# Optimization experiments

Hardware: AMD Instinct MI355X
Metric: run time of the kernel (lower is better)

The kernel has to match this reference:

```python
import jax, jax.numpy as jnp
import numpy as np

TIME_GAP_BUCKETS = 64
B, L, H, MAX_T = 256, 200, 256, 256
VOCAB, N_GROUPS = 50000, 16
EPS = 1e-5


def setup_inputs() -> dict:
    key = jax.random.key(0)
    ks = jax.random.split(key, 16)
    lengths = jax.random.randint(ks[0], (B,), 0, L + 1)
    mask = jnp.arange(L)[None, :] < lengths[:, None]

    def toks(k, hi):  # jagged padded-dense: zeros past each row's length
        return jnp.where(mask, jax.random.randint(k, (B, L), 0, hi), 0)

    inp = {
        'history_tokens': toks(ks[1], VOCAB),
        'history_post_tokens': toks(ks[2], VOCAB),
        'history_author_tokens': toks(ks[3], VOCAB),
        'history_action_tokens': toks(ks[4], VOCAB),
        'history_time_gap': toks(ks[5], TIME_GAP_BUCKETS + 1),
        'history_group_ids': jnp.where(mask, jnp.sort(jax.random.randint(ks[6], (B, L), 1, N_GROUPS + 1), axis=1), 0),
        'lengths': lengths,
    }
    s = 0.02
    inp['token_emb'] = jax.random.normal(ks[7], (VOCAB, H)) * s
    inp['ln_gamma'] = jnp.ones((6 * H,))
    inp['ln_beta'] = jnp.zeros((6 * H,))
    inp['w1'] = jax.random.normal(ks[8], (6 * H, 4 * H)) * (1.0 / np.sqrt(6 * H)).astype(np.float32)
    inp['b1'] = jnp.zeros((4 * H,))
    inp['w2'] = jax.random.normal(ks[9], (4 * H, H)) * (1.0 / np.sqrt(4 * H)).astype(np.float32)
    inp['b2'] = jnp.zeros((H,))
    inp['time_gap_emb'] = (jax.random.normal(ks[10], (TIME_GAP_BUCKETS + 1, H)) * s).at[0].set(0.0)  # padding_idx=0
    inp['group_emb'] = (jax.random.normal(ks[11], (N_GROUPS + 1, H)) * s).at[0].set(0.0)  # padding_idx=0
    inp['pos_emb'] = jax.random.normal(ks[12], (MAX_T, H)) * s
    inp['sep_token'] = jax.random.normal(ks[13], (H,)) * 0.02
    return inp


def _layernorm(x, g, b):
    mu = jnp.mean(x, axis=-1, keepdims=True)
    var = jnp.mean(jnp.square(x - mu), axis=-1, keepdims=True)
    return (x - mu) * jax.lax.rsqrt(var + EPS) * g + b


def _merge_with_sep(event_tokens, group_ids, mask, sep_token):
    # mask is a prefix mask (positions < lengths), so valid tokens are contiguous.
    Bn, Ln, Hn = event_tokens.shape
    next_mask = jnp.pad(mask[:, 1:], ((0, 0), (0, 1)))
    next_group = jnp.pad(group_ids[:, 1:], ((0, 0), (0, 1)))
    sep_after = mask & next_mask & (group_ids != next_group)  # insert sep after token i
    seps_before = jnp.cumsum(sep_after, axis=1) - sep_after.astype(jnp.int32)  # exclusive scan
    token_pos = jnp.arange(Ln)[None, :] + seps_before  # position within merged piece list
    total = mask.sum(axis=1) + sep_after.sum(axis=1)  # [B] merged piece count
    offset = MAX_T - total  # right-align; negative -> leading pieces dropped
    tok_idx = offset[:, None] + token_pos
    sep_idx = tok_idx + 1
    tok_idx = jnp.where(mask & (tok_idx >= 0), tok_idx, MAX_T)  # MAX_T => dropped
    sep_idx = jnp.where(sep_after & (sep_idx >= 0), sep_idx, MAX_T)
    sep_rows = jnp.broadcast_to(sep_token, (Ln, Hn))

    def scatter_one(ev, ti, si):
        buf = jnp.zeros((MAX_T, Hn), ev.dtype)
        buf = buf.at[ti].set(ev, mode='drop')
        buf = buf.at[si].set(sep_rows, mode='drop')
        return buf

    merged = jax.vmap(scatter_one)(event_tokens, tok_idx, sep_idx)
    merged_len = jnp.minimum(total, MAX_T)
    merged_mask = jnp.arange(MAX_T)[None, :] >= (MAX_T - merged_len)[:, None]
    return merged, merged_mask


def reference(history_tokens, history_post_tokens, history_author_tokens,
              history_action_tokens, history_time_gap, history_group_ids,
              lengths, token_emb, ln_gamma, ln_beta, w1, b1, w2, b2,
              time_gap_emb, group_emb, pos_emb, sep_token):
    mask = jnp.arange(L)[None, :] < lengths[:, None]
    hh = token_emb[history_tokens]
    ph = token_emb[history_post_tokens]
    ah = token_emb[history_author_tokens]
    ch = token_emb[history_action_tokens]
    th = time_gap_emb[jnp.clip(history_time_gap, 0, TIME_GAP_BUCKETS)]
    gh = group_emb[history_group_ids]
    ev = jnp.concatenate([hh, ph, ah, ch, th, gh], axis=-1)  # [B, L, 6H]
    x = _layernorm(ev, ln_gamma, ln_beta)
    x = jax.nn.silu(x @ w1 + b1)  # dropout is identity in eval mode
    event_tokens = x @ w2 + b2  # [B, L, H]
    merged, mm = _merge_with_sep(event_tokens, history_group_ids, mask, sep_token)
    merged = (merged + pos_emb[None]) * mm[..., None].astype(merged.dtype)
    return merged, mm
```

## Files before the change

### kernel.cpp

```cpp
#include <hip/hip_runtime.h>
#include <hip/hip_bf16.h>
#include <math.h>

#define B_    256
#define L_    200
#define H_    256
#define MAXT  256
#define SIXH  1536
#define FOURH 1024
#define NPOS  (B_ * L_)

typedef __attribute__((ext_vector_type(8))) short short8;
typedef __attribute__((ext_vector_type(4))) float f32x4;

typedef __attribute__((address_space(3))) void lds_void;
typedef const __attribute__((address_space(1))) void gbl_void;

#define ASM_BAR() asm volatile("s_barrier" ::: "memory")
#define VMCNT4()  asm volatile("s_waitcnt vmcnt(4)" ::: "memory")
#define VMCNT0()  asm volatile("s_waitcnt vmcnt(0)" ::: "memory")

__global__ void scan_offsets(const int* __restrict__ lengths,
                             int* __restrict__ offsets) {
  if (threadIdx.x == 0) {
    int acc = 0;
    for (int b = 0; b < B_; b++) { offsets[b] = acc; acc += lengths[b]; }
    offsets[B_] = acc;
  }
}

__global__ void zero_pad_x(__hip_bfloat16* __restrict__ x,
                           const int* __restrict__ offsets) {
  int total = offsets[B_];
  int padded = (total + 255) & ~255;
  int row = total + blockIdx.x;
  if (row >= padded) return;
  int t = threadIdx.x;
#pragma unroll
  for (int j = 0; j < 6; j++)
    x[(size_t)row * SIXH + j * 256 + t] = __float2bfloat16(0.0f);
}

__global__ void tpos_kernel(const int* __restrict__ gids,
                            const int* __restrict__ lengths,
                            const int* __restrict__ offsets,
                            int* __restrict__ tpos) {
  int b = blockIdx.x;
  if (threadIdx.x != 0) return;
  int len = lengths[b];
  int base = offsets[b];
  const int* g = gids + b * L_;
  int nsep = 0;
  for (int l = 0; l + 1 < len; l++)
    if (g[l] != g[l + 1]) nsep++;
  int total = len + nsep;
  int off = MAXT - total;
  int sb = 0;
  for (int l = 0; l < len; l++) {
    int ti = off + l + sb;
    tpos[base + l] = (ti >= 0) ? (b * MAXT + ti) : -1;
    if (l + 1 < len && g[l] != g[l + 1]) sb++;
  }
}

__global__ void transpose_to_bf16(const float* __restrict__ in,
                                  __hip_bfloat16* __restrict__ out,
                                  int R, int C) {
  __shared__ float tile[32][33];
  int tc = blockIdx.x, tr = blockIdx.y;
  int tx = threadIdx.x & 31, ty = threadIdx.x >> 5;
#pragma unroll
  for (int i = 0; i < 4; i++) {
    int r = tr * 32 + ty + i * 8;
    int c = tc * 32 + tx;
    tile[ty + i * 8][tx] = in[(size_t)r * C + c];
  }
  __syncthreads();
#pragma unroll
  for (int i = 0; i < 4; i++) {
    int orow = tc * 32 + ty + i * 8;
    int ocol = tr * 32 + tx;
    out[(size_t)orow * R + ocol] = __float2bfloat16(tile[tx][ty + i * 8]);
  }
}

__global__ void embed_ln_kernel(const int* __restrict__ tok0,
                                const int* __restrict__ tok1,
                                const int* __restrict__ tok2,
                                const int* __restrict__ tok3,
                                const int* __restrict__ tgap,
                                const int* __restrict__ gid,
                                const int* __restrict__ lengths,
                                const int* __restrict__ offsets,
                                const float* __restrict__ token_emb,
                                const float* __restrict__ tg_emb,
                                const float* __restrict__ g_emb,
                                const float* __restrict__ gamma,
                                const float* __restrict__ beta,
                                __hip_bfloat16* __restrict__ xout) {
  int l = blockIdx.x, b = blockIdx.y;
  if (l >= lengths[b]) return;
  int pos = b * L_ + l;
  int row = offsets[b] + l;
  int t = threadIdx.x;
  int wv = t >> 6;
  int ln = t & 63;
  int c4 = ln * 4;

  const float* tab;
  int idx;
  if (wv == 0)      { tab = token_emb; idx = tok0[pos]; }
  else if (wv == 1) { tab = token_emb; idx = tok1[pos]; }
  else if (wv == 2) { tab = token_emb; idx = tok2[pos]; }
  else if (wv == 3) { tab = token_emb; idx = tok3[pos]; }
  else if (wv == 4) { tab = tg_emb;    idx = min(max(tgap[pos], 0), 64); }
  else              { tab = g_emb;     idx = gid[pos]; }

  float4 v = *(const float4*)&tab[(size_t)idx * H_ + c4];

  float s = v.x + v.y + v.z + v.w;
  float q = v.x * v.x + v.y * v.y + v.z * v.z + v.w * v.w;
#pragma unroll
  for (int o = 32; o; o >>= 1) { s += __shfl_down(s, o); q += __shfl_down(q, o); }
  __shared__ float ps[6], pq[6];
  if (ln == 0) { ps[wv] = s; pq[wv] = q; }
  __syncthreads();
  float ts = 0.f, tq = 0.f;
#pragma unroll
  for (int k = 0; k < 6; k++) { ts += ps[k]; tq += pq[k]; }
  float mu = ts * (1.0f / 1536.0f);
  float var = tq * (1.0f / 1536.0f) - mu * mu;
  float rstd = rsqrtf(var + 1e-5f);

  int cbase = wv * 256 + c4;
  float4 gm = *(const float4*)&gamma[cbase];
  float4 bt = *(const float4*)&beta[cbase];
  float y0 = (v.x - mu) * rstd * gm.x + bt.x;
  float y1 = (v.y - mu) * rstd * gm.y + bt.y;
  float y2 = (v.z - mu) * rstd * gm.z + bt.z;
  float y3 = (v.w - mu) * rstd * gm.w + bt.w;
  __hip_bfloat16 h0 = __float2bfloat16(y0), h1 = __float2bfloat16(y1);
  __hip_bfloat16 h2 = __float2bfloat16(y2), h3 = __float2bfloat16(y3);
  ushort4 pk;
  pk.x = *(unsigned short*)&h0; pk.y = *(unsigned short*)&h1;
  pk.z = *(unsigned short*)&h2; pk.w = *(unsigned short*)&h3;
  *(ushort4*)&xout[(size_t)row * SIXH + cbase] = pk;
}

__global__ __launch_bounds__(512, 2)
void gemm1_8ph(const __hip_bfloat16* __restrict__ A,
               const __hip_bfloat16* __restrict__ Bt,
               const float* __restrict__ bias,
               __hip_bfloat16* __restrict__ out,
               const int* __restrict__ total_ptr) {
  constexpr int K = SIXH;
  constexpr int NT = K / 64;
  constexpr int N = FOURH;

  extern __shared__ __align__(16) char lds[];

  int total = total_ptr[0];
  int padded = (total + 255) & ~255;

  int flat = blockIdx.y * 4 + blockIdx.x;
  int xcd = flat & 7, idx = flat >> 3;
  int mt = (idx >> 2) * 8 + xcd;
  int nt = idx & 3;
  int m0 = mt * 256;
  int n0 = nt * 256;
  if (m0 >= padded) return;

  int tid = threadIdx.x;
  int lane = tid & 63;
  int w = tid >> 6;
  int wave_m = w >> 2;
  int wave_n = w & 3;

  int r15 = lane & 15, g = lane >> 4;
  int slot_r = (((r15 & 1) << 2) | g) ^ (r15 >> 1);
  int lane_off = (r15 >> 1) * 128 + slot_r * 16;

  int s0 = (tid & 7) ^ ((tid >> 3) & 7);
  int scol = (s0 & 3) * 8;
  int row0 = ((tid >> 3) << 1) + (s0 >> 2);
  int ldst0 = w * 1024;

#define REGA(d, h) (lds + (d) * 65536 + (h) * 16384)
#define REGB(d, h) (lds + (d) * 65536 + 32768 + (h) * 16384)

#define STAGE(P, t0, kt, h, rb)                                                \
  do {                                                                         \
    __builtin_amdgcn_global_load_lds(                                          \
        (gbl_void*)((P) + (size_t)((t0) + row0) * K + (kt) * 64 + (h) * 32 +   \
                    scol),                                                     \
        (lds_void*)((rb) + ldst0), 16, 0, 0);                                  \
    __builtin_amdgcn_global_load_lds(                                          \
        (gbl_void*)((P) + (size_t)((t0) + row0 + 128) * K + (kt) * 64 +        \
                    (h) * 32 + scol),                                          \
        (lds_void*)((rb) + 8192 + ldst0), 16, 0, 0);                           \
  } while (0)

  f32x4 acc[8][4] = {};

  STAGE(A, m0, 0, 0, REGA(0, 0));
  STAGE(Bt, n0, 0, 0, REGB(0, 0));
  STAGE(A, m0, 0, 1, REGA(0, 1));
  STAGE(Bt, n0, 0, 1, REGB(0, 1));
  STAGE(A, m0, 1, 0, REGA(1, 0));
  STAGE(Bt, n0, 1, 0, REGB(1, 0));
  VMCNT4();
  ASM_BAR();

  for (int kt = 0; kt < NT; ++kt) {
    int d = kt & 1;
    int kc1 = (kt + 1 < NT) ? kt + 1 : NT - 1;
    int kc2 = (kt + 2 < NT) ? kt + 2 : NT - 1;
    char* A0 = REGA(d, 0); char* A1 = REGA(d, 1);
    char* B0 = REGB(d, 0); char* B1 = REGB(d, 1);
    char* An1 = REGA(d ^ 1, 1);
    char* Bn1 = REGB(d ^ 1, 1);

    short8 a[4], b[4];

#pragma unroll
    for (int ni = 0; ni < 4; ni++)
      b[ni] = *(const short8*)(B0 + (wave_n * 64 + ni * 16) * 64 + lane_off);
#pragma unroll
    for (int j = 0; j < 4; j++)
      a[j] = *(const short8*)(A0 + (wave_m * 128 + j * 16) * 64 + lane_off);
    STAGE(A, m0, kc1, 1, An1);
    ASM_BAR();
    __builtin_amdgcn_s_setprio(1);
#pragma unroll
    for (int j = 0; j < 4; j++)
#pragma unroll
      for (int ni = 0; ni < 4; ni++)
        acc[j][ni] =
            __builtin_amdgcn_mfma_f32_16x16x32_bf16(a[j], b[ni], acc[j][ni], 0, 0, 0);
    __builtin_amdgcn_s_setprio(0);
    ASM_BAR();

#pragma unroll
    for (int j = 0; j < 4; j++)
      a[j] = *(const short8*)(A0 + (wave_m * 128 + (4 + j) * 16) * 64 + lane_off);
    STAGE(Bt, n0, kc1, 1, Bn1);
    ASM_BAR();
    __builtin_amdgcn_s_setprio(1);
#pragma unroll
    for (int j = 0; j < 4; j++)
#pragma unroll
      for (int ni = 0; ni < 4; ni++)
        acc[4 + j][ni] =
            __builtin_amdgcn_mfma_f32_16x16x32_bf16(a[j], b[ni], acc[4 + j][ni], 0, 0, 0);
    __builtin_amdgcn_s_setprio(0);
    ASM_BAR();

#pragma unroll
    for (int ni = 0; ni < 4; ni++)
      b[ni] = *(const short8*)(B1 + (wave_n * 64 + ni * 16) * 64 + lane_off);
#pragma unroll
    for (int j = 0; j < 4; j++)
      a[j] = *(const short8*)(A1 + (wave_m * 128 + j * 16) * 64 + lane_off);
    STAGE(A, m0, kc2, 0, A0);
    ASM_BAR();
    __builtin_amdgcn_s_setprio(1);
#pragma unroll
    for (int j = 0; j < 4; j++)
#pragma unroll
      for (int ni = 0; ni < 4; ni++)
        acc[j][ni] =
            __builtin_amdgcn_mfma_f32_16x16x32_bf16(a[j], b[ni], acc[j][ni], 0, 0, 0);
    __builtin_amdgcn_s_setprio(0);
    ASM_BAR();

#pragma unroll
    for (int j = 0; j < 4; j++)
      a[j] = *(const short8*)(A1 + (wave_m * 128 + (4 + j) * 16) * 64 + lane_off);
    STAGE(Bt, n0, kc2, 0, B0);
    ASM_BAR();
    __builtin_amdgcn_s_setprio(1);
#pragma unroll
    for (int j = 0; j < 4; j++)
#pragma unroll
      for (int ni = 0; ni < 4; ni++)
        acc[4 + j][ni] =
            __builtin_amdgcn_mfma_f32_16x16x32_bf16(a[j], b[ni], acc[4 + j][ni], 0, 0, 0);
    __builtin_amdgcn_s_setprio(0);
    VMCNT4();
    ASM_BAR();
  }
  VMCNT0();

  int r0 = g * 4;
  int cc = r15;
#pragma unroll
  for (int mi = 0; mi < 8; mi++)
#pragma unroll
    for (int ni = 0; ni < 4; ni++) {
      int col = n0 + wave_n * 64 + ni * 16 + cc;
      float bv = bias[col];
#pragma unroll
      for (int r = 0; r < 4; r++) {
        int row = m0 + wave_m * 128 + mi * 16 + r0 + r;
        float v = acc[mi][ni][r] + bv;
        v = v / (1.0f + __expf(-v));
        out[(size_t)row * N + col] = __float2bfloat16(v);
      }
    }
#undef STAGE
#undef REGA
#undef REGB
}

__global__ void gemm2_scatter(const __hip_bfloat16* __restrict__ A,
                              const __hip_bfloat16* __restrict__ Bt,
                              const float* __restrict__ bias,
                              const int* __restrict__ tpos,
                              const float* __restrict__ pos_emb,
                              float* __restrict__ out,
                              const int* __restrict__ total_ptr,
                              int N, int K) {
  int m0 = blockIdx.y * 128;
  int total = total_ptr[0];
  int padded = (total + 127) & ~127;
  if (m0 >= padded) return;

  __shared__ __hip_bfloat16 As[128 * 64];
  __shared__ __hip_bfloat16 Bs[128 * 64];
  int n0 = blockIdx.x * 128;
  int tid = threadIdx.x;
  int lane = tid & 63, wid = tid >> 6;
  int wm = (wid >> 1) * 64, wn = (wid & 1) * 64;

  int srow = (lane >> 3);
  int scol = (lane & 7) * 8;

  f32x4 acc[4][4] = {};

  for (int k0 = 0; k0 < K; k0 += 64) {
#pragma unroll
    for (int i = 0; i < 4; i++) {
      int c = wid * 4 + i;
      int row = c * 8 + srow;
      __builtin_amdgcn_global_load_lds(
          (gbl_void*)&A[(size_t)(m0 + row) * K + k0 + scol],
          (lds_void*)(As + c * 512), 16, 0, 0);
      __builtin_amdgcn_global_load_lds(
          (gbl_void*)&Bt[(size_t)(n0 + row) * K + k0 + scol],
          (lds_void*)(Bs + c * 512), 16, 0, 0);
    }
    __syncthreads();
#pragma unroll
    for (int kk = 0; kk < 64; kk += 32) {
      short8 a[4], bb[4];
#pragma unroll
      for (int m = 0; m < 4; m++)
        a[m] = *(const short8*)&As[(wm + m * 16 + (lane & 15)) * 64 + kk +
                                   8 * (lane >> 4)];
#pragma unroll
      for (int n = 0; n < 4; n++)
        bb[n] = *(const short8*)&Bs[(wn + n * 16 + (lane & 15)) * 64 + kk +
                                    8 * (lane >> 4)];
#pragma unroll
      for (int m = 0; m < 4; m++)
#pragma unroll
        for (int n = 0; n < 4; n++)
          acc[m][n] = __builtin_amdgcn_mfma_f32_16x16x32_bf16(a[m], bb[n],
                                                              acc[m][n], 0, 0, 0);
    }
    __syncthreads();
  }

  int r0 = (lane >> 4) * 4;
  int cc = lane & 15;
#pragma unroll
  for (int m = 0; m < 4; m++) {
#pragma unroll
    for (int r = 0; r < 4; r++) {
      int row = m0 + wm + m * 16 + r0 + r;
      if (row >= total) continue;
      int pa = tpos[row];
      if (pa < 0) continue;
      int p = pa & (MAXT - 1);
#pragma unroll
      for (int n = 0; n < 4; n++) {
        int col = n0 + wn + n * 16 + cc;
        float v = acc[m][n][r] + bias[col] + pos_emb[p * H_ + col];
        out[(size_t)pa * H_ + col] = v;
      }
    }
  }
}

__global__ void merge2_kernel(const int* __restrict__ gids,
                              const int* __restrict__ lengths,
                              const float* __restrict__ sep_token,
                              const float* __restrict__ pos_emb,
                              float* __restrict__ out) {
  int b = blockIdx.x, t = threadIdx.x;
  __shared__ signed char src[MAXT];
  __shared__ int g[L_];
  __shared__ int sh_total;
  int len = lengths[b];
  src[t] = 0;
  for (int l = t; l < len; l += 256) g[l] = gids[b * L_ + l];
  __syncthreads();
  if (t == 0) {
    int nsep = 0;
    for (int l = 0; l + 1 < len; l++)
      if (g[l] != g[l + 1]) nsep++;
    int total = len + nsep;
    sh_total = total;
    int off = MAXT - total;
    int sb = 0;
    for (int l = 0; l < len; l++) {
      int ti = off + l + sb;
      if (ti >= 0) src[ti] = 2;
      if (l + 1 < len && g[l] != g[l + 1]) {
        if (ti + 1 >= 0) src[ti + 1] = 1;
        sb++;
      }
    }
  }
  __syncthreads();
  int total = sh_total;
  int mlen = min(total, MAXT);

  int q = t >> 6, lane = t & 63, c4 = lane * 4;
  float4 sep4 = *(const float4*)&sep_token[c4];
  float* orow = out + (size_t)b * MAXT * H_;
  for (int p0 = 0; p0 < MAXT; p0 += 4) {
    int p = p0 + q;
    int s = src[p];
    if (s == 2) continue;
    float4 v;
    if (s == 1) {
      float4 pe = *(const float4*)&pos_emb[p * H_ + c4];
      v.x = sep4.x + pe.x; v.y = sep4.y + pe.y;
      v.z = sep4.z + pe.z; v.w = sep4.w + pe.w;
    } else {
      v.x = 0.f; v.y = 0.f; v.z = 0.f; v.w = 0.f;
    }
    *(float4*)&orow[(size_t)p * H_ + c4] = v;
  }
  float* mm = out + (size_t)B_ * MAXT * H_;
  mm[b * MAXT + t] = (t >= MAXT - mlen) ? 1.0f : 0.0f;
}

extern "C" void kernel_launch(void* const* d_in, const int* in_sizes, int n_in,
                              void* d_out, int out_size, void* d_ws,
                              size_t ws_size, hipStream_t stream) {
  const int* tok0 = (const int*)d_in[0];
  const int* tok1 = (const int*)d_in[1];
  const int* tok2 = (const int*)d_in[2];
  const int* tok3 = (const int*)d_in[3];
  const int* tgap = (const int*)d_in[4];
  const int* gid  = (const int*)d_in[5];
  const int* lengths = (const int*)d_in[6];
  const float* token_emb = (const float*)d_in[7];
  const float* gamma = (const float*)d_in[8];
  const float* beta  = (const float*)d_in[9];
  const float* w1 = (const float*)d_in[10];
  const float* b1 = (const float*)d_in[11];
  const float* w2 = (const float*)d_in[12];
  const float* b2 = (const float*)d_in[13];
  const float* tg_emb = (const float*)d_in[14];
  const float* g_emb  = (const float*)d_in[15];
  const float* pos_emb = (const float*)d_in[16];
  const float* sep_tok = (const float*)d_in[17];

  const size_t NEEDED = 265815044;
  if (ws_size < NEEDED) return;

  char* ws = (char*)d_ws;
  __hip_bfloat16* x = (__hip_bfloat16*)ws;
  int* tpos = (int*)ws;
  __hip_bfloat16* h = (__hip_bfloat16*)(ws + 157286400);
  __hip_bfloat16* w1t = (__hip_bfloat16*)(ws + 262144000);
  __hip_bfloat16* w2t = (__hip_bfloat16*)(ws + 265289728);
  int* offsets = (int*)(ws + 265814016);

  scan_offsets<<<1, 64, 0, stream>>>(lengths, offsets);
  zero_pad_x<<<256, 256, 0, stream>>>(x, offsets);

  transpose_to_bf16<<<dim3(1024 / 32, 1536 / 32), 256, 0, stream>>>(w1, w1t,
                                                                    1536, 1024);
  transpose_to_bf16<<<dim3(256 / 32, 1024 / 32), 256, 0, stream>>>(w2, w2t,
                                                                   1024, 256);

  embed_ln_kernel<<<dim3(L_, B_), 384, 0, stream>>>(
      tok0, tok1, tok2, tok3, tgap, gid, lengths, offsets, token_emb, tg_emb,
      g_emb, gamma, beta, x);

  hipFuncSetAttribute((const void*)gemm1_8ph,
                      hipFuncAttributeMaxDynamicSharedMemorySize, 131072);
  gemm1_8ph<<<dim3(4, NPOS / 256), 512, 131072, stream>>>(x, w1t, b1, h,
                                                          offsets + B_);

  tpos_kernel<<<B_, 64, 0, stream>>>(gid, lengths, offsets, tpos);

  gemm2_scatter<<<dim3(H_ / 128, NPOS / 128), 256, 0, stream>>>(
      h, w2t, b2, tpos, pos_emb, (float*)d_out, offsets + B_, H_, FOURH);

  merge2_kernel<<<B_, 256, 0, stream>>>(gid, lengths, sep_tok, pos_emb,
                                        (float*)d_out);
}
```

Before: 258.4 us.

## Make GEMM1 persistent over M tiles and stage group ids in LDS for tpos

GEMM1 now launches a fixed grid of 256 blocks that loop over the M tiles of the valid rows with stride 64. Each block keeps a fixed N tile and hoists the bias loads out of the tile loop. This removes the many early-exit blocks of the old 4x200 grid and the cost of launching them, and gives the blocks a steady schedule. The tpos kernel also loads each row's group ids into shared memory with 64 threads before the single-thread serial scan. The risks are tail imbalance when the M-tile count does not divide evenly, and dropping the old XCD-aware tile mapping, which may reduce L2 reuse.

```diff
diff --git a/kernel.cpp b/kernel.cpp
--- a/kernel.cpp
+++ b/kernel.cpp
@@ -45,11 +45,13 @@
                             const int* __restrict__ lengths,
                             const int* __restrict__ offsets,
                             int* __restrict__ tpos) {
-  int b = blockIdx.x;
-  if (threadIdx.x != 0) return;
+  int b = blockIdx.x, t = threadIdx.x;
+  __shared__ int g[L_];
   int len = lengths[b];
+  for (int l = t; l < len; l += 64) g[l] = gids[b * L_ + l];
+  __syncthreads();
+  if (t != 0) return;
   int base = offsets[b];
-  const int* g = gids + b * L_;
   int nsep = 0;
   for (int l = 0; l + 1 < len; l++)
     if (g[l] != g[l + 1]) nsep++;
@@ -161,14 +163,12 @@
 
   int total = total_ptr[0];
   int padded = (total + 255) & ~255;
-
-  int flat = blockIdx.y * 4 + blockIdx.x;
-  int xcd = flat & 7, idx = flat >> 3;
-  int mt = (idx >> 2) * 8 + xcd;
-  int nt = idx & 3;
-  int m0 = mt * 256;
+  int num_mt = padded >> 8;
+
+  int bid = blockIdx.x;
+  int nt = (bid & 7) >> 1;
+  int local = ((bid >> 3) << 1) | (bid & 1);
   int n0 = nt * 256;
-  if (m0 >= padded) return;
 
   int tid = threadIdx.x;
   int lane = tid & 63;
@@ -184,6 +184,11 @@
   int scol = (s0 & 3) * 8;
   int row0 = ((tid >> 3) << 1) + (s0 >> 2);
   int ldst0 = w * 1024;
+
+  float bv4[4];
+#pragma unroll
+  for (int ni = 0; ni < 4; ni++)
+    bv4[ni] = bias[n0 + wave_n * 64 + ni * 16 + r15];
 
 #define REGA(d, h) (lds + (d) * 65536 + (h) * 16384)
 #define REGB(d, h) (lds + (d) * 65536 + 32768 + (h) * 16384)
@@ -200,113 +205,116 @@
         (lds_void*)((rb) + 8192 + ldst0), 16, 0, 0);                           \
   } while (0)
 
-  f32x4 acc[8][4] = {};
-
-  STAGE(A, m0, 0, 0, REGA(0, 0));
-  STAGE(Bt, n0, 0, 0, REGB(0, 0));
-  STAGE(A, m0, 0, 1, REGA(0, 1));
-  STAGE(Bt, n0, 0, 1, REGB(0, 1));
-  STAGE(A, m0, 1, 0, REGA(1, 0));
-  STAGE(Bt, n0, 1, 0, REGB(1, 0));
-  VMCNT4();
-  ASM_BAR();
-
-  for (int kt = 0; kt < NT; ++kt) {
-    int d = kt & 1;
-    int kc1 = (kt + 1 < NT) ? kt + 1 : NT - 1;
-    int kc2 = (kt + 2 < NT) ? kt + 2 : NT - 1;
-    char* A0 = REGA(d, 0); char* A1 = REGA(d, 1);
-    char* B0 = REGB(d, 0); char* B1 = REGB(d, 1);
-    char* An1 = REGA(d ^ 1, 1);
-    char* Bn1 = REGB(d ^ 1, 1);
-
-    short8 a[4], b[4];
-
-#pragma unroll
-    for (int ni = 0; ni < 4; ni++)
-      b[ni] = *(const short8*)(B0 + (wave_n * 64 + ni * 16) * 64 + lane_off);
-#pragma unroll
-    for (int j = 0; j < 4; j++)
-      a[j] = *(const short8*)(A0 + (wave_m * 128 + j * 16) * 64 + lane_off);
-    STAGE(A, m0, kc1, 1, An1);
-    ASM_BAR();
-    __builtin_amdgcn_s_setprio(1);
-#pragma unroll
-    for (int j = 0; j < 4; j++)
-#pragma unroll
-      for (int ni = 0; ni < 4; ni++)
-        acc[j][ni] =
-            __builtin_amdgcn_mfma_f32_16x16x32_bf16(a[j], b[ni], acc[j][ni], 0, 0, 0);
-    __builtin_amdgcn_s_setprio(0);
-    ASM_BAR();
-
-#pragma unroll
-    for (int j = 0; j < 4; j++)
-      a[j] = *(const short8*)(A0 + (wave_m * 128 + (4 + j) * 16) * 64 + lane_off);
-    STAGE(Bt, n0, kc1, 1, Bn1);
-    ASM_BAR();
-    __builtin_amdgcn_s_setprio(1);
-#pragma unroll
-    for (int j = 0; j < 4; j++)
-#pragma unroll
-      for (int ni = 0; ni < 4; ni++)
-        acc[4 + j][ni] =
-            __builtin_amdgcn_mfma_f32_16x16x32_bf16(a[j], b[ni], acc[4 + j][ni], 0, 0, 0);
-    __builtin_amdgcn_s_setprio(0);
-    ASM_BAR();
-
-#pragma unroll
-    for (int ni = 0; ni < 4; ni++)
-      b[ni] = *(const short8*)(B1 + (wave_n * 64 + ni * 16) * 64 + lane_off);
-#pragma unroll
-    for (int j = 0; j < 4; j++)
-      a[j] = *(const short8*)(A1 + (wave_m * 128 + j * 16) * 64 + lane_off);
-    STAGE(A, m0, kc2, 0, A0);
-    ASM_BAR();
-    __builtin_amdgcn_s_setprio(1);
-#pragma unroll
-    for (int j = 0; j < 4; j++)
-#pragma unroll
-      for (int ni = 0; ni < 4; ni++)
-        acc[j][ni] =
-            __builtin_amdgcn_mfma_f32_16x16x32_bf16(a[j], b[ni], acc[j][ni], 0, 0, 0);
-    __builtin_amdgcn_s_setprio(0);
-    ASM_BAR();
-
-#pragma unroll
-    for (int j = 0; j < 4; j++)
-      a[j] = *(const short8*)(A1 + (wave_m * 128 + (4 + j) * 16) * 64 + lane_off);
-    STAGE(Bt, n0, kc2, 0, B0);
-    ASM_BAR();
-    __builtin_amdgcn_s_setprio(1);
-#pragma unroll
-    for (int j = 0; j < 4; j++)
-#pragma unroll
-      for (int ni = 0; ni < 4; ni++)
-        acc[4 + j][ni] =
-            __builtin_amdgcn_mfma_f32_16x16x32_bf16(a[j], b[ni], acc[4 + j][ni], 0, 0, 0);
-    __builtin_amdgcn_s_setprio(0);
+  for (int mt = local; mt < num_mt; mt += 64) {
+    int m0 = mt * 256;
+
+    f32x4 acc[8][4] = {};
+
+    STAGE(A, m0, 0, 0, REGA(0, 0));
+    STAGE(Bt, n0, 0, 0, REGB(0, 0));
+    STAGE(A, m0, 0, 1, REGA(0, 1));
+    STAGE(Bt, n0, 0, 1, REGB(0, 1));
+    STAGE(A, m0, 1, 0, REGA(1, 0));
+    STAGE(Bt, n0, 1, 0, REGB(1, 0));
     VMCNT4();
     ASM_BAR();
-  }
-  VMCNT0();
-
-  int r0 = g * 4;
-  int cc = r15;
-#pragma unroll
-  for (int mi = 0; mi < 8; mi++)
-#pragma unroll
-    for (int ni = 0; ni < 4; ni++) {
-      int col = n0 + wave_n * 64 + ni * 16 + cc;
-      float bv = bias[col];
-#pragma unroll
-      for (int r = 0; r < 4; r++) {
-        int row = m0 + wave_m * 128 + mi * 16 + r0 + r;
-        float v = acc[mi][ni][r] + bv;
-        v = v / (1.0f + __expf(-v));
-        out[(size_t)row * N + col] = __float2bfloat16(v);
+
+    for (int kt = 0; kt < NT; ++kt) {
+      int d = kt & 1;
+      int kc1 = (kt + 1 < NT) ? kt + 1 : NT - 1;
+      int kc2 = (kt + 2 < NT) ? kt + 2 : NT - 1;
+      char* A0 = REGA(d, 0); char* A1 = REGA(d, 1);
+      char* B0 = REGB(d, 0); char* B1 = REGB(d, 1);
+      char* An1 = REGA(d ^ 1, 1);
+      char* Bn1 = REGB(d ^ 1, 1);
+
+      short8 a[4], b[4];
+
+#pragma unroll
+      for (int ni = 0; ni < 4; ni++)
+        b[ni] = *(const short8*)(B0 + (wave_n * 64 + ni * 16) * 64 + lane_off);
+#pragma unroll
+      for (int j = 0; j < 4; j++)
+        a[j] = *(const short8*)(A0 + (wave_m * 128 + j * 16) * 64 + lane_off);
+      STAGE(A, m0, kc1, 1, An1);
+      ASM_BAR();
+      __builtin_amdgcn_s_setprio(1);
+#pragma unroll
+      for (int j = 0; j < 4; j++)
+#pragma unroll
+        for (int ni = 0; ni < 4; ni++)
+          acc[j][ni] = __builtin_amdgcn_mfma_f32_16x16x32_bf16(a[j], b[ni],
+                                                               acc[j][ni], 0, 0, 0);
+      __builtin_amdgcn_s_setprio(0);
+      ASM_BAR();
+
+#pragma unroll
+      for (int j = 0; j < 4; j++)
+        a[j] = *(const short8*)(A0 + (wave_m * 128 + (4 + j) * 16) * 64 + lane_off);
+      STAGE(Bt, n0, kc1, 1, Bn1);
+      ASM_BAR();
+      __builtin_amdgcn_s_setprio(1);
+#pragma unroll
+      for (int j = 0; j < 4; j++)
+#pragma unroll
+        for (int ni = 0; ni < 4; ni++)
+          acc[4 + j][ni] = __builtin_amdgcn_mfma_f32_16x16x32_bf16(
+              a[j], b[ni], acc[4 + j][ni], 0, 0, 0);
+      __builtin_amdgcn_s_setprio(0);
+      ASM_BAR();
+
+#pragma unroll
+      for (int ni = 0; ni < 4; ni++)
+        b[ni] = *(const short8*)(B1 + (wave_n * 64 + ni * 16) * 64 + lane_off);
+#pragma unroll
+      for (int j = 0; j < 4; j++)
+        a[j] = *(const short8*)(A1 + (wave_m * 128 + j * 16) * 64 + lane_off);
+      STAGE(A, m0, kc2, 0, A0);
+      ASM_BAR();
+      __builtin_amdgcn_s_setprio(1);
+#pragma unroll
+      for (int j = 0; j < 4; j++)
+#pragma unroll
+        for (int ni = 0; ni < 4; ni++)
+          acc[j][ni] = __builtin_amdgcn_mfma_f32_16x16x32_bf16(a[j], b[ni],
+                                                               acc[j][ni], 0, 0, 0);
+      __builtin_amdgcn_s_setprio(0);
+      ASM_BAR();
+
+#pragma unroll
+      for (int j = 0; j < 4; j++)
+        a[j] = *(const short8*)(A1 + (wave_m * 128 + (4 + j) * 16) * 64 + lane_off);
+      STAGE(Bt, n0, kc2, 0, B0);
+      ASM_BAR();
+      __builtin_amdgcn_s_setprio(1);
+#pragma unroll
+      for (int j = 0; j < 4; j++)
+#pragma unroll
+        for (int ni = 0; ni < 4; ni++)
+          acc[4 + j][ni] = __builtin_amdgcn_mfma_f32_16x16x32_bf16(
+              a[j], b[ni], acc[4 + j][ni], 0, 0, 0);
+      __builtin_amdgcn_s_setprio(0);
+      VMCNT4();
+      ASM_BAR();
+    }
+    VMCNT0();
+
+    int r0 = g * 4;
+#pragma unroll
+    for (int mi = 0; mi < 8; mi++)
+#pragma unroll
+      for (int ni = 0; ni < 4; ni++) {
+        int col = n0 + wave_n * 64 + ni * 16 + r15;
+        float bv = bv4[ni];
+#pragma unroll
+        for (int r = 0; r < 4; r++) {
+          int row = m0 + wave_m * 128 + mi * 16 + r0 + r;
+          float v = acc[mi][ni][r] + bv;
+          v = v / (1.0f + __expf(-v));
+          out[(size_t)row * N + col] = __float2bfloat16(v);
+        }
       }
-    }
+  }
 #undef STAGE
 #undef REGA
 #undef REGB
@@ -494,8 +502,7 @@
 
   hipFuncSetAttribute((const void*)gemm1_8ph,
                       hipFuncAttributeMaxDynamicSharedMemorySize, 131072);
-  gemm1_8ph<<<dim3(4, NPOS / 256), 512, 131072, stream>>>(x, w1t, b1, h,
-                                                          offsets + B_);
+  gemm1_8ph<<<256, 512, 131072, stream>>>(x, w1t, b1, h, offsets + B_);
 
   tpos_kernel<<<B_, 64, 0, stream>>>(gid, lengths, offsets, tpos);
 
```

Result: no change. 259.1 us (+0.3%).
